# Optimization experiments

Measured on AMD Instinct MI355X. Metric: run time of the kernel, lower is better.

## Reference

```python
import jax, jax.numpy as jnp
import numpy as np
import math

EMBED_DIM = 1024
NUM_HEADS = 16
HEAD_DIM = EMBED_DIM // NUM_HEADS
SEQ = 1024
BATCH = 8


def setup_inputs() -> dict:
    key = jax.random.key(0)
    k1, k2, k3, k4, k5 = jax.random.split(key, 5)
    q = jax.random.normal(k1, (SEQ, BATCH, EMBED_DIM), dtype=jnp.float32)
    # module asserts key == query (self-attention only)
    in_proj_w = jax.random.normal(k2, (3 * EMBED_DIM, EMBED_DIM), dtype=jnp.float32) * 0.02
    in_proj_b = jax.random.normal(k3, (3 * EMBED_DIM,), dtype=jnp.float32) * 0.02
    out_proj_w = jax.random.normal(k4, (EMBED_DIM, EMBED_DIM), dtype=jnp.float32) * 0.02
    out_proj_b = jax.random.normal(k5, (EMBED_DIM,), dtype=jnp.float32) * 0.02
    return {
        "query": q,
        "key": q,
        "value": q,
        "in_proj_w": in_proj_w,
        "in_proj_b": in_proj_b,
        "out_proj_w": out_proj_w,
        "out_proj_b": out_proj_b,
    }


def reference(query, key, value, in_proj_w, in_proj_b, out_proj_w, out_proj_b):
    s, b, e = query.shape
    nh, hd = NUM_HEADS, HEAD_DIM
    norm = math.sqrt(hd)
    # fused QKV projection: [s, b, 3e]
    mixed = query @ in_proj_w.T + in_proj_b
    mixed = mixed.reshape(s, b, nh, 3 * hd)
    q, k, v = jnp.split(mixed, 3, axis=-1)  # each [s, b, nh, hd]
    # -> [b*nh, s, hd]
    q = q.reshape(s, b * nh, hd).transpose(1, 0, 2) / norm
    k = k.reshape(s, b * nh, hd).transpose(1, 0, 2)
    v = v.reshape(s, b * nh, hd).transpose(1, 0, 2)
    # full O(s^2) attention matrix, as in the original bmm/softmax/bmm
    scores = jnp.einsum('nqd,nkd->nqk', q, k)  # [b*nh, s, s]
    probs = jax.nn.softmax(scores, axis=-1)
    ctx = jnp.einsum('nqk,nkd->nqd', probs, v)  # [b*nh, s, hd]
    # [b*nh, s, hd] -> [s, b, e]
    ctx = ctx.reshape(b, nh, s, hd).transpose(2, 0, 1, 3).reshape(s, b, e)
    return ctx @ out_proj_w.T + out_proj_b
```

## Files before the change

kernel.cpp:

```cpp
#include <hip/hip_runtime.h>

typedef __bf16 bf16_t;
typedef __bf16 bf16x4 __attribute__((ext_vector_type(4)));
typedef __bf16 bf16x8 __attribute__((ext_vector_type(8)));
typedef float f32x4 __attribute__((ext_vector_type(4)));

#define MFMA16(a, b, c) __builtin_amdgcn_mfma_f32_16x16x32_bf16((a), (b), (c), 0, 0, 0)

__device__ __forceinline__ const bf16_t* tile_ptr(const bf16_t* t, int row, int kchunk) {
    return t + row * 64 + (((kchunk ^ (row & 7))) << 3);
}

__device__ __forceinline__ void stage64(const bf16_t* __restrict__ gbase, size_t gstride,
                                        bf16_t* lds_rowbase, int lane) {
    const int rr = lane >> 3, cl = lane & 7;
    const bf16_t* g = gbase + (size_t)rr * gstride + ((cl ^ rr) << 3);
    __builtin_amdgcn_global_load_lds((__attribute__((address_space(1))) const void*)g,
                                     (__attribute__((address_space(3))) void*)lds_rowbase,
                                     16, 0, 0);
}

__device__ __forceinline__ int cs_addr(int m, int n) {
    return m * 128 + ((((n >> 3) ^ ((m >> 3) & 7))) << 3) + (n & 7);
}

__global__ void __launch_bounds__(256) k_cvt(
    const float* __restrict__ q, const float* __restrict__ wi, const float* __restrict__ wo,
    bf16_t* __restrict__ qb, bf16_t* __restrict__ wib, bf16_t* __restrict__ wob)
{
    const int g = blockIdx.x * 256 + threadIdx.x;
    const float* src; bf16_t* dst; int off;
    if (g < 1048576)      { src = q;  dst = qb;  off = g; }
    else if (g < 1441792) { src = wi; dst = wib; off = g - 1048576; }
    else                  { src = wo; dst = wob; off = g - 1441792; }
    const float4* s4 = (const float4*)(src + (size_t)off * 8);
    float4 a = s4[0], b = s4[1];
    bf16x8 v;
    v[0] = (bf16_t)a.x; v[1] = (bf16_t)a.y; v[2] = (bf16_t)a.z; v[3] = (bf16_t)a.w;
    v[4] = (bf16_t)b.x; v[5] = (bf16_t)b.y; v[6] = (bf16_t)b.z; v[7] = (bf16_t)b.w;
    *(bf16x8*)(dst + (size_t)off * 8) = v;
}

__global__ void __launch_bounds__(256) k_qkv(
    const bf16_t* __restrict__ A, const bf16_t* __restrict__ W,
    const float* __restrict__ bias,
    bf16_t* __restrict__ Qh, bf16_t* __restrict__ Kh, bf16_t* __restrict__ Vt)
{
    __shared__ bf16_t smem[16384];
    bf16_t* As = smem;
    bf16_t* Bs = smem + 8192;
    const int m0 = blockIdx.x * 128;
    const int n0 = blockIdx.y * 128;
    const int which = n0 >> 10;
    const int hbase = (n0 & 1023) >> 6;
    const int t = threadIdx.x;
    const int wave = t >> 6, lane = t & 63;
    const int quad = lane >> 4, l16 = lane & 15;
    const int wm = (wave & 1) * 64, wn = (wave >> 1) * 64;

    f32x4 acc[4][4] = {};

    for (int k0 = 0; k0 < 1024; k0 += 64) {
        __syncthreads();
        #pragma unroll
        for (int p = 0; p < 4; ++p) {
            const int rb = wave * 32 + p * 8;
            stage64(A + (size_t)(m0 + rb) * 1024 + k0, 1024, As + rb * 64, lane);
            const int np = n0 + rb;
            const int wrow = ((np & 1023) >> 6) * 192 + which * 64 + (np & 63);
            stage64(W + (size_t)wrow * 1024 + k0, 1024, Bs + rb * 64, lane);
        }
        __syncthreads();
        #pragma unroll
        for (int ks = 0; ks < 2; ++ks) {
            bf16x8 af[4], bf[4];
            #pragma unroll
            for (int i = 0; i < 4; ++i)
                af[i] = *(const bf16x8*)tile_ptr(As, wm + i * 16 + l16, ks * 4 + quad);
            #pragma unroll
            for (int j = 0; j < 4; ++j)
                bf[j] = *(const bf16x8*)tile_ptr(Bs, wn + j * 16 + l16, ks * 4 + quad);
            #pragma unroll
            for (int i = 0; i < 4; ++i)
                #pragma unroll
                for (int j = 0; j < 4; ++j)
                    acc[i][j] = MFMA16(af[i], bf[j], acc[i][j]);
        }
    }

    __syncthreads();
    const float scale = (which == 0) ? 0.180336880111112f : 1.0f;
    #pragma unroll
    for (int j = 0; j < 4; ++j) {
        const int nl = wn + j * 16 + l16;
        const float bv = bias[(hbase + (nl >> 6)) * 192 + which * 64 + (nl & 63)];
        #pragma unroll
        for (int i = 0; i < 4; ++i) {
            #pragma unroll
            for (int rg = 0; rg < 4; ++rg) {
                const int ml = wm + i * 16 + quad * 4 + rg;
                smem[cs_addr(ml, nl)] = (bf16_t)((acc[i][j][rg] + bv) * scale);
            }
        }
    }
    __syncthreads();

    const int si0 = m0 >> 3;
    if (which < 2) {
        bf16_t* dst = which ? Kh : Qh;
        #pragma unroll
        for (int u = 0; u < 4; ++u) {
            const int unit = wave * 4 + u;
            const int h = unit >> 3, bi = unit & 7;
            const int head = bi * 16 + hbase + h;
            #pragma unroll
            for (int pass = 0; pass < 2; ++pass) {
                const int si = pass * 8 + (lane >> 3);
                const int dc = lane & 7;
                const int ml = si * 8 + bi;
                const int nch = (h * 8 + dc) ^ (si & 7);
                bf16x8 v = *(const bf16x8*)&smem[ml * 128 + nch * 8];
                *(bf16x8*)(dst + (size_t)head * 65536 + (size_t)(si0 + si) * 64 + dc * 8) = v;
            }
        }
    } else {
        #pragma unroll
        for (int u = 0; u < 8; ++u) {
            const int unit = wave * 8 + u;
            const int h = unit >> 4, bi = (unit >> 1) & 7, c = unit & 1;
            const int head = bi * 16 + hbase + h;
            const int d = lane;
            bf16x8 v;
            #pragma unroll
            for (int e = 0; e < 8; ++e) {
                const int ml = (c * 8 + e) * 8 + bi;
                const int nch = (h * 8 + (d >> 3)) ^ e;
                v[e] = smem[ml * 128 + nch * 8 + (d & 7)];
            }
            *(bf16x8*)(Vt + (size_t)head * 65536 +
                       (size_t)(si0 / 8 + c) * 512 + (size_t)d * 8) = v;
        }
    }
}

__global__ void __launch_bounds__(256, 4) k_attn(
    const bf16_t* __restrict__ Qh, const bf16_t* __restrict__ Kh,
    const bf16_t* __restrict__ Vg, bf16_t* __restrict__ Ctx)
{
    __shared__ bf16_t Pw[4][32 * 64];

    const int bid = blockIdx.x;
    const int head = (bid & 7) * 16 + ((bid >> 3) & 15);
    const int qt = bid >> 7;
    const int t = threadIdx.x;
    const int wave = t >> 6, lane = t & 63;
    const int quad = lane >> 4, l16 = lane & 15;

    const bf16_t* Qg = Qh + (size_t)head * 65536 + (size_t)qt * 8192;
    const bf16_t* Kg = Kh + (size_t)head * 65536;
    const bf16_t* Vgh = Vg + (size_t)head * 65536;

    bf16x8 qf[2][2];
    #pragma unroll
    for (int half = 0; half < 2; ++half)
        #pragma unroll
        for (int ks = 0; ks < 2; ++ks)
            qf[half][ks] = *(const bf16x8*)(
                Qg + (size_t)(wave * 32 + half * 16 + l16) * 64 + ks * 32 + quad * 8);

    bf16x8 ones;
    #pragma unroll
    for (int e = 0; e < 8; ++e) ones[e] = (bf16_t)((l16 == 0) ? 1.0f : 0.0f);

    f32x4 vacc[2][5] = {};

    for (int kt = 0; kt < 16; ++kt) {
        f32x4 s[2][4] = {};
        #pragma unroll
        for (int ks = 0; ks < 2; ++ks) {
            #pragma unroll
            for (int j = 0; j < 4; ++j) {
                bf16x8 kf = *(const bf16x8*)(
                    Kg + (size_t)(kt * 64 + j * 16 + l16) * 64 + (ks * 4 + quad) * 8);
                s[0][j] = MFMA16(kf, qf[0][ks], s[0][j]);
                s[1][j] = MFMA16(kf, qf[1][ks], s[1][j]);
            }
        }

        #pragma unroll
        for (int half = 0; half < 2; ++half) {
            const int row = half * 16 + l16;
            #pragma unroll
            for (int j = 0; j < 4; ++j) {
                bf16x4 pv;
                #pragma unroll
                for (int rg = 0; rg < 4; ++rg)
                    pv[rg] = (bf16_t)exp2f(s[half][j][rg]);
                const int chunk = j * 2 + (quad >> 1);
                *(bf16x4*)&Pw[wave][row * 64 + ((chunk ^ (row & 7)) << 3) + (quad & 1) * 4] = pv;
            }
        }
        asm volatile("s_waitcnt lgkmcnt(0)" ::: "memory");

        #pragma unroll
        for (int ks = 0; ks < 2; ++ks) {
            bf16x8 pf0 = *(const bf16x8*)tile_ptr(Pw[wave], l16, ks * 4 + quad);
            bf16x8 pf1 = *(const bf16x8*)tile_ptr(Pw[wave], 16 + l16, ks * 4 + quad);
            #pragma unroll
            for (int n = 0; n < 4; ++n) {
                bf16x8 vf = *(const bf16x8*)(
                    Vgh + (size_t)(kt * 8 + ks * 4 + quad) * 512 + (n * 16 + l16) * 8);
                vacc[0][n] = MFMA16(pf0, vf, vacc[0][n]);
                vacc[1][n] = MFMA16(pf1, vf, vacc[1][n]);
            }
            vacc[0][4] = MFMA16(pf0, ones, vacc[0][4]);
            vacc[1][4] = MFMA16(pf1, ones, vacc[1][4]);
        }
    }

    const int bi = head >> 4, h = head & 15;
    #pragma unroll
    for (int half = 0; half < 2; ++half) {
        #pragma unroll
        for (int rg = 0; rg < 4; ++rg) {
            const float l = __shfl(vacc[half][4][rg], lane & 48, 64);
            const float inv = 1.0f / l;
            const int si = qt * 128 + wave * 32 + half * 16 + quad * 4 + rg;
            #pragma unroll
            for (int n = 0; n < 4; ++n)
                Ctx[((size_t)si * 8 + bi) * 1024 + h * 64 + n * 16 + l16] =
                    (bf16_t)(vacc[half][n][rg] * inv);
        }
    }
}

__global__ void __launch_bounds__(256) k_out(
    const bf16_t* __restrict__ A, const bf16_t* __restrict__ W,
    const float* __restrict__ bias, float* __restrict__ out)
{
    __shared__ bf16_t As[128 * 64];
    __shared__ bf16_t Bs[128 * 64];
    const int m0 = blockIdx.x * 128;
    const int n0 = blockIdx.y * 128;
    const int t = threadIdx.x;
    const int wave = t >> 6, lane = t & 63;
    const int quad = lane >> 4, l16 = lane & 15;
    const int wm = (wave & 1) * 64, wn = (wave >> 1) * 64;

    f32x4 acc[4][4] = {};

    for (int k0 = 0; k0 < 1024; k0 += 64) {
        __syncthreads();
        #pragma unroll
        for (int p = 0; p < 4; ++p) {
            const int rb = wave * 32 + p * 8;
            stage64(A + (size_t)(m0 + rb) * 1024 + k0, 1024, As + rb * 64, lane);
            stage64(W + (size_t)(n0 + rb) * 1024 + k0, 1024, Bs + rb * 64, lane);
        }
        __syncthreads();
        #pragma unroll
        for (int ks = 0; ks < 2; ++ks) {
            bf16x8 af[4], bf[4];
            #pragma unroll
            for (int i = 0; i < 4; ++i)
                af[i] = *(const bf16x8*)tile_ptr(As, wm + i * 16 + l16, ks * 4 + quad);
            #pragma unroll
            for (int j = 0; j < 4; ++j)
                bf[j] = *(const bf16x8*)tile_ptr(Bs, wn + j * 16 + l16, ks * 4 + quad);
            #pragma unroll
            for (int i = 0; i < 4; ++i)
                #pragma unroll
                for (int j = 0; j < 4; ++j)
                    acc[i][j] = MFMA16(af[i], bf[j], acc[i][j]);
        }
    }

    #pragma unroll
    for (int j = 0; j < 4; ++j) {
        const int n = n0 + wn + j * 16 + l16;
        const float bv = bias[n];
        #pragma unroll
        for (int i = 0; i < 4; ++i) {
            #pragma unroll
            for (int rg = 0; rg < 4; ++rg) {
                const int m = m0 + wm + i * 16 + quad * 4 + rg;
                out[(size_t)m * 1024 + n] = acc[i][j][rg] + bv;
            }
        }
    }
}

extern "C" void kernel_launch(void* const* d_in, const int* in_sizes, int n_in,
                              void* d_out, int out_size, void* d_ws, size_t ws_size,
                              hipStream_t stream)
{
    const float* query = (const float*)d_in[0];
    const float* in_w  = (const float*)d_in[3];
    const float* in_b  = (const float*)d_in[4];
    const float* out_w = (const float*)d_in[5];
    const float* out_b = (const float*)d_in[6];
    float* out = (float*)d_out;

    bf16_t* Wi  = (bf16_t*)d_ws;
    bf16_t* Wo  = Wi + (size_t)3145728;
    bf16_t* Qh  = Wo + (size_t)1048576;
    bf16_t* Kh  = Qh + (size_t)8388608;
    bf16_t* Vt  = Kh + (size_t)8388608;
    bf16_t* Aq  = Vt + (size_t)8388608;
    bf16_t* Ctx = Aq;

    k_cvt<<<dim3(6144), 256, 0, stream>>>(query, in_w, out_w, Aq, Wi, Wo);
    k_qkv<<<dim3(64, 24), 256, 0, stream>>>(Aq, Wi, in_b, Qh, Kh, Vt);
    k_attn<<<dim3(1024), 256, 0, stream>>>(Qh, Kh, Vt, Ctx);
    k_out<<<dim3(64, 8), 256, 0, stream>>>(Ctx, Wo, out_b, out);
}
```

Measured before the change: 305.3 us.

## Double-buffer K tiles in LDS via async global_load_lds and prefetch V fragments

K tiles are now staged cooperatively into a double-buffered shared-memory array with async global-to-LDS loads, so the next tile is prefetched while the current one is consumed and all four waves share one copy. V fragments are loaded into registers before the softmax/P write so their global latency overlaps the exp work. This adds a block-wide barrier per tile, extra LDS use (which may lower occupancy under the 4-block launch bound), and higher register pressure from the held V fragments.

After: 278.7 us. -8.7%, faster.

```diff
diff --git a/kernel.cpp b/kernel.cpp
--- a/kernel.cpp
+++ b/kernel.cpp
@@ -147,6 +147,7 @@
     const bf16_t* __restrict__ Qh, const bf16_t* __restrict__ Kh,
     const bf16_t* __restrict__ Vg, bf16_t* __restrict__ Ctx)
 {
+    __shared__ bf16_t Ks[2][64 * 64];
     __shared__ bf16_t Pw[4][32 * 64];
 
     const int bid = blockIdx.x;
@@ -174,49 +175,79 @@
 
     f32x4 vacc[2][5] = {};
 
-    for (int kt = 0; kt < 16; ++kt) {
-        f32x4 s[2][4] = {};
-        #pragma unroll
-        for (int ks = 0; ks < 2; ++ks) {
-            #pragma unroll
-            for (int j = 0; j < 4; ++j) {
-                bf16x8 kf = *(const bf16x8*)(
-                    Kg + (size_t)(kt * 64 + j * 16 + l16) * 64 + (ks * 4 + quad) * 8);
-                s[0][j] = MFMA16(kf, qf[0][ks], s[0][j]);
-                s[1][j] = MFMA16(kf, qf[1][ks], s[1][j]);
-            }
-        }
-
-        #pragma unroll
-        for (int half = 0; half < 2; ++half) {
-            const int row = half * 16 + l16;
-            #pragma unroll
-            for (int j = 0; j < 4; ++j) {
-                bf16x4 pv;
-                #pragma unroll
-                for (int rg = 0; rg < 4; ++rg)
-                    pv[rg] = (bf16_t)exp2f(s[half][j][rg]);
-                const int chunk = j * 2 + (quad >> 1);
-                *(bf16x4*)&Pw[wave][row * 64 + ((chunk ^ (row & 7)) << 3) + (quad & 1) * 4] = pv;
-            }
-        }
-        asm volatile("s_waitcnt lgkmcnt(0)" ::: "memory");
-
-        #pragma unroll
-        for (int ks = 0; ks < 2; ++ks) {
-            bf16x8 pf0 = *(const bf16x8*)tile_ptr(Pw[wave], l16, ks * 4 + quad);
-            bf16x8 pf1 = *(const bf16x8*)tile_ptr(Pw[wave], 16 + l16, ks * 4 + quad);
-            #pragma unroll
-            for (int n = 0; n < 4; ++n) {
-                bf16x8 vf = *(const bf16x8*)(
-                    Vgh + (size_t)(kt * 8 + ks * 4 + quad) * 512 + (n * 16 + l16) * 8);
-                vacc[0][n] = MFMA16(pf0, vf, vacc[0][n]);
-                vacc[1][n] = MFMA16(pf1, vf, vacc[1][n]);
-            }
-            vacc[0][4] = MFMA16(pf0, ones, vacc[0][4]);
-            vacc[1][4] = MFMA16(pf1, ones, vacc[1][4]);
-        }
-    }
+    #pragma unroll
+    for (int p = 0; p < 2; ++p) {
+        const int rb = wave * 16 + p * 8;
+        stage64(Kg + (size_t)rb * 64, 64, Ks[0] + rb * 64, lane);
+    }
+
+#define KT_BODY(CUR, NXT, KT, DO_ST)                                          \
+    {                                                                         \
+        __syncthreads();                                                      \
+        if (DO_ST) {                                                          \
+            _Pragma("unroll")                                                 \
+            for (int p = 0; p < 2; ++p) {                                     \
+                const int rb = wave * 16 + p * 8;                             \
+                stage64(Kg + (size_t)(((KT) + 1) * 64 + rb) * 64, 64,         \
+                        (NXT) + rb * 64, lane);                               \
+            }                                                                 \
+        }                                                                     \
+        f32x4 s[2][4] = {};                                                   \
+        _Pragma("unroll")                                                     \
+        for (int ks = 0; ks < 2; ++ks) {                                      \
+            _Pragma("unroll")                                                 \
+            for (int j = 0; j < 4; ++j) {                                     \
+                bf16x8 kf = *(const bf16x8*)tile_ptr((CUR), j * 16 + l16,     \
+                                                     ks * 4 + quad);          \
+                s[0][j] = MFMA16(kf, qf[0][ks], s[0][j]);                     \
+                s[1][j] = MFMA16(kf, qf[1][ks], s[1][j]);                     \
+            }                                                                 \
+        }                                                                     \
+        bf16x8 vf[2][4];                                                      \
+        _Pragma("unroll")                                                     \
+        for (int ks = 0; ks < 2; ++ks)                                        \
+            _Pragma("unroll")                                                 \
+            for (int n = 0; n < 4; ++n)                                       \
+                vf[ks][n] = *(const bf16x8*)(                                 \
+                    Vgh + (size_t)((KT) * 8 + ks * 4 + quad) * 512            \
+                        + (n * 16 + l16) * 8);                                \
+        _Pragma("unroll")                                                     \
+        for (int half = 0; half < 2; ++half) {                                \
+            const int row = half * 16 + l16;                                  \
+            _Pragma("unroll")                                                 \
+            for (int j = 0; j < 4; ++j) {                                     \
+                bf16x4 pv;                                                    \
+                _Pragma("unroll")                                             \
+                for (int rg = 0; rg < 4; ++rg)                                \
+                    pv[rg] = (bf16_t)exp2f(s[half][j][rg]);                   \
+                const int chunk = j * 2 + (quad >> 1);                        \
+                *(bf16x4*)&Pw[wave][row * 64 + ((chunk ^ (row & 7)) << 3)     \
+                                    + (quad & 1) * 4] = pv;                   \
+            }                                                                 \
+        }                                                                     \
+        asm volatile("s_waitcnt lgkmcnt(0)" ::: "memory");                    \
+        _Pragma("unroll")                                                     \
+        for (int ks = 0; ks < 2; ++ks) {                                      \
+            bf16x8 pf0 = *(const bf16x8*)tile_ptr(Pw[wave], l16,              \
+                                                  ks * 4 + quad);             \
+            bf16x8 pf1 = *(const bf16x8*)tile_ptr(Pw[wave], 16 + l16,         \
+                                                  ks * 4 + quad);             \
+            _Pragma("unroll")                                                 \
+            for (int n = 0; n < 4; ++n) {                                     \
+                vacc[0][n] = MFMA16(pf0, vf[ks][n], vacc[0][n]);              \
+                vacc[1][n] = MFMA16(pf1, vf[ks][n], vacc[1][n]);              \
+            }                                                                 \
+            vacc[0][4] = MFMA16(pf0, ones, vacc[0][4]);                       \
+            vacc[1][4] = MFMA16(pf1, ones, vacc[1][4]);                       \
+        }                                                                     \
+    }
+
+    #pragma unroll 1
+    for (int it = 0; it < 8; ++it) {
+        KT_BODY(Ks[0], Ks[1], 2 * it, true);
+        KT_BODY(Ks[1], Ks[0], 2 * it + 1, it < 7);
+    }
+#undef KT_BODY
 
     const int bi = head >> 4, h = head & 15;
     #pragma unroll
```
